# Kernel tuning notes

Hardware: AMD Instinct MI355X
Metric: run time of the kernel (lower is better)

Reference implementation:

```python
import jax, jax.numpy as jnp
import numpy as np

N, S, E, H = 8, 1024, 1024, 16
DK = E // H

def setup_inputs() -> dict:
    key = jax.random.key(0)
    ks = jax.random.split(key, 10)
    s = 1.0 / np.sqrt(E)
    x = jax.random.normal(ks[0], (N, S, E), dtype=jnp.float32)
    attn_mask = jax.random.randint(ks[1], (N, S, S), 0, 2) == 1
    Wq = jax.random.normal(ks[2], (E, E), dtype=jnp.float32) * s
    Wk = jax.random.normal(ks[3], (E, E), dtype=jnp.float32) * s
    Wv = jax.random.normal(ks[4], (E, E), dtype=jnp.float32) * s
    Wo = jax.random.normal(ks[5], (E, E), dtype=jnp.float32) * s
    bq = jax.random.normal(ks[6], (E,), dtype=jnp.float32) * s
    bk = jax.random.normal(ks[7], (E,), dtype=jnp.float32) * s
    bv = jax.random.normal(ks[8], (E,), dtype=jnp.float32) * s
    bo = jax.random.normal(ks[9], (E,), dtype=jnp.float32) * s
    return {"x": x, "attn_mask": attn_mask, "Wq": Wq, "bq": bq, "Wk": Wk, "bk": bk,
            "Wv": Wv, "bv": bv, "Wo": Wo, "bo": bo}

def reference(x, attn_mask, Wq, bq, Wk, bk, Wv, bv, Wo, bo):
    n, s, e = x.shape
    # projections, split into heads: (N, H, S, DK)
    q = (x @ Wq + bq).reshape(n, s, H, DK).transpose(0, 2, 1, 3)
    k = (x @ Wk + bk).reshape(n, s, H, DK).transpose(0, 2, 1, 3)
    v = (x @ Wv + bv).reshape(n, s, H, DK).transpose(0, 2, 1, 3)
    logits = jnp.einsum("nhqd,nhkd->nhqk", q, k) / np.sqrt(DK).astype(np.float32)
    # mask==True positions are suppressed (masked_fill with -1e9)
    logits = jnp.where(attn_mask[:, None, :, :], jnp.float32(-1e9), logits)
    attn = jax.nn.softmax(logits, axis=-1)  # exp(log_softmax) == softmax
    o = jnp.einsum("nhqk,nhkd->nhqd", attn, v)
    o = o.transpose(0, 2, 1, 3).reshape(n, s, e)
    return o @ Wo + bo
```

## Files before the change

kernel.cpp:

```cpp
#include <hip/hip_runtime.h>
#include <hip/hip_bf16.h>

typedef unsigned short u16;
typedef unsigned int   u32;
typedef unsigned long long u64;

#define SEQ 1024
#define EMB 1024
#define NH  16
#define DKH 64

#define QSCALE 0.18033688f
#define SCLAMP 43.3f

typedef __attribute__((ext_vector_type(8))) short short8;
typedef __attribute__((ext_vector_type(4))) float floatx4;

__device__ __forceinline__ float b2f(u16 u) {
  return __uint_as_float(((u32)u) << 16);
}
__device__ __forceinline__ u16 f2b(float f) {
  u32 u = __float_as_uint(f);
  u32 r = u + 0x7fffu + ((u >> 16) & 1u);
  return (u16)(r >> 16);
}

__device__ __forceinline__ void glds16(const u16* g, u16* l) {
  __builtin_amdgcn_global_load_lds(
      (const __attribute__((address_space(1))) u32*)g,
      (__attribute__((address_space(3))) u32*)l, 16, 0, 0);
}

__global__ __launch_bounds__(256) void probe_inputs(const u32* __restrict__ A,
                                                    const u32* __restrict__ B,
                                                    int* __restrict__ flags) {
  __shared__ int mA, mB, mBig, xB16;
  if (threadIdx.x == 0) { mA = 0; mB = 0; mBig = 0; xB16 = 0; }
  __syncthreads();
  int la = 0, lb = 0;
  for (int i = threadIdx.x; i < 4096; i += 256) {
    if ((A[i] & 0xFEFEFEFEu) == 0) la++;
    if ((B[i] & 0xFEFEFEFEu) == 0) lb++;
  }
  atomicAdd(&mA, la); atomicAdd(&mB, lb);
  __syncthreads();
  const int xIsB = (mA > mB) ? 1 : 0;
  const u32* X = xIsB ? B : A;
  const u32* M = xIsB ? A : B;
  int big = 0, cnt = 0;
  for (int i = threadIdx.x; i < 4096; i += 256)
    if (M[i] > 1u) big = 1;
  for (int i = threadIdx.x; i < 2048; i += 256) {
    u16 v = (u16)(X[i] & 0xffffu);
    int e = (v >> 7) & 0xFF;
    if (e >= 110 && e <= 135) cnt++;
  }
  if (big) atomicOr(&mBig, 1);
  atomicAdd(&xB16, cnt);
  __syncthreads();
  if (threadIdx.x == 0) {
    flags[0] = xIsB;
    flags[1] = (xB16 > 1500) ? 1 : 0;
    flags[2] = mBig;
  }
}

__global__ __launch_bounds__(256) void convert_x(const void* __restrict__ bigA,
                                                 const void* __restrict__ bigB,
                                                 const int* __restrict__ flags,
                                                 u16* __restrict__ out) {
  const void* x = flags[0] ? bigB : bigA;
  int i = (blockIdx.x * 256 + threadIdx.x) * 4;
  if (flags[1]) {
    *(ushort4*)(out + i) = *(const ushort4*)((const u16*)x + i);
  } else {
    float4 v = *(const float4*)((const float*)x + i);
    ushort4 o;
    o.x = f2b(v.x); o.y = f2b(v.y); o.z = f2b(v.z); o.w = f2b(v.w);
    *(ushort4*)(out + i) = o;
  }
}

__global__ __launch_bounds__(256) void build_maskbits(const void* __restrict__ bigA,
                                                      const void* __restrict__ bigB,
                                                      const int* __restrict__ flags,
                                                      u32* __restrict__ out) {
  const void* mask = flags[0] ? bigA : bigB;
  const int mbyte = flags[2];
  const int t = threadIdx.x;
  const int lane = t & 63, w = t >> 6;
  const u64 base0 = (u64)blockIdx.x * 8192;
#pragma unroll 4
  for (int k = 0; k < 32; k++) {
    u64 idx = base0 + k * 256 + t;
    int v;
    if (mbyte) v = ((const unsigned char*)mask)[idx] == 0;
    else       v = ((const u32*)mask)[idx] == 0;
    u64 b = __ballot(v);
    if (lane == 0) {
      u64 wbase = (base0 + k * 256 + w * 64) >> 5;
      out[wbase]     = (u32)b;
      out[wbase + 1] = (u32)(b >> 32);
    }
  }
}

__global__ __launch_bounds__(256) void transpose_convert_w4(
    const void* __restrict__ w0, const void* __restrict__ w1,
    const void* __restrict__ w2, const void* __restrict__ w3,
    u16* __restrict__ outQKV, u16* __restrict__ outO,
    const int* __restrict__ flags) {
  __shared__ float tile[32][33];
  const int z = blockIdx.z;
  const void* in = (z == 0) ? w0 : (z == 1) ? w1 : (z == 2) ? w2 : w3;
  u16* out = (z < 3) ? (outQKV + (u64)z * EMB * EMB) : outO;
  const float scale = (z == 0) ? QSCALE : 1.0f;
  const int amode = flags[1];
  const int tx = threadIdx.x & 31;
  const int ty = threadIdx.x >> 5;
  const int bx = blockIdx.x * 32, by = blockIdx.y * 32;
  if (amode) {
    const u16* inb = (const u16*)in;
#pragma unroll
    for (int r = ty; r < 32; r += 8)
      tile[r][tx] = b2f(inb[(u64)(by + r) * EMB + bx + tx]);
  } else {
    const float* inf = (const float*)in;
#pragma unroll
    for (int r = ty; r < 32; r += 8)
      tile[r][tx] = inf[(u64)(by + r) * EMB + bx + tx];
  }
  __syncthreads();
#pragma unroll
  for (int r = ty; r < 32; r += 8)
    out[(u64)(bx + r) * EMB + by + tx] = f2b(tile[tx][r] * scale);
}

__global__ __launch_bounds__(256) void convert_biases(const void* b0, const void* b1,
                                                      const void* b2, const void* b3,
                                                      float* __restrict__ out,
                                                      const int* __restrict__ flags) {
  const void* ptrs[4] = {b0, b1, b2, b3};
  const void* p = ptrs[blockIdx.x];
  const float scale = (blockIdx.x == 0) ? QSCALE : 1.0f;
  const int amode = flags[1];
  for (int i = threadIdx.x; i < 1024; i += 256) {
    float v = amode ? b2f(((const u16*)p)[i]) : ((const float*)p)[i];
    out[blockIdx.x * 1024 + i] = v * scale;
  }
}

#define VTP 65
__global__ __launch_bounds__(256) void transpose_v(const u16* __restrict__ in,
                                                   u16* __restrict__ out) {
  __shared__ u16 tile[64 * VTP];
  const int t = threadIdx.x;
  const int s0 = blockIdx.x * 64;
  const u64 off = (u64)blockIdx.y * SEQ * DKH;
  const int row = t >> 2, c0 = (t & 3) * 16;
  const u16* ip = in + off + (u64)(s0 + row) * DKH + c0;
  *(uint4*)(&tile[row * VTP + c0])     = *(const uint4*)(ip);
  *(uint4*)(&tile[row * VTP + c0 + 8]) = *(const uint4*)(ip + 8);
  __syncthreads();
  const int d = t >> 2;
  u16 buf[16];
#pragma unroll
  for (int j = 0; j < 16; j++) buf[j] = tile[(c0 + j) * VTP + d];
  u16* op = out + off + (u64)d * SEQ + s0 + c0;
  *(uint4*)(op)     = *(uint4*)(&buf[0]);
  *(uint4*)(op + 8) = *(uint4*)(&buf[8]);
}


template <int OUTMODE>
__device__ __forceinline__ void gemm_core(
    const u16* __restrict__ X, const u16* __restrict__ Wt,
    const float* __restrict__ bias,
    u16* __restrict__ Qg, u16* __restrict__ Kg, u16* __restrict__ Vh,
    float* __restrict__ outf, int row0) {
  __shared__ __align__(16) u16 lds[2][(256 + 128) * 64];
  const int t = threadIdx.x;
  const int lane = t & 63;
  const int w = t >> 6;
  const int wr = w >> 1, wc = w & 1;
  const int l15 = lane & 15, l4 = lane >> 4;
  const int bM = blockIdx.x * 256, bN = blockIdx.y * 128;
  const int r7 = l15 & 7;
  const int cA = (l4 ^ r7) << 3;
  const int cB = (l4 ^ r7 ^ 4) << 3;

  floatx4 acc[4][4];
#pragma unroll
  for (int i = 0; i < 4; i++)
#pragma unroll
    for (int j = 0; j < 4; j++)
      acc[i][j] = (floatx4){0.f, 0.f, 0.f, 0.f};

  const int srow = w * 8 + (lane >> 3);
  const int schk = ((lane & 7) ^ (lane >> 3)) << 3;
  const u16* Ap = X + (u64)(row0 + bM + srow) * EMB + schk;
  const u16* Bp = Wt + (u64)(bN + srow) * EMB + schk;
  u16* Ad0 = &lds[0][w * 512];
  u16* Bd0 = &lds[0][16384 + w * 512];
  u16* Ad1 = &lds[1][w * 512];
  u16* Bd1 = &lds[1][16384 + w * 512];

  auto stage = [&](u16* Ad, u16* Bd, int k0) {
    glds16(Ap + k0, Ad);
    glds16(Ap + k0 + 64 * EMB, Ad + 4096);
    glds16(Ap + k0 + 128 * EMB, Ad + 8192);
    glds16(Ap + k0 + 192 * EMB, Ad + 12288);
    glds16(Bp + k0, Bd);
    glds16(Bp + k0 + 64 * EMB, Bd + 4096);
  };

  auto compute = [&](const u16* __restrict__ Ab, const u16* __restrict__ Bb) {
    short8 bf[4][2];
#pragma unroll
    for (int n = 0; n < 4; n++) {
      const int gr = (wc * 64 + n * 16 + l15) * 64;
      bf[n][0] = *(const short8*)(&Bb[gr + cA]);
      bf[n][1] = *(const short8*)(&Bb[gr + cB]);
    }
#pragma unroll
    for (int mh = 0; mh < 2; mh++) {
      short8 af[2][2];
#pragma unroll
      for (int m = 0; m < 2; m++) {
        const int fr = (wr * 64 + mh * 32 + m * 16 + l15) * 64;
        af[m][0] = *(const short8*)(&Ab[fr + cA]);
        af[m][1] = *(const short8*)(&Ab[fr + cB]);
      }
      __builtin_amdgcn_s_setprio(1);
#pragma unroll
      for (int m = 0; m < 2; m++)
#pragma unroll
        for (int n = 0; n < 4; n++) {
          acc[mh * 2 + m][n] = __builtin_amdgcn_mfma_f32_16x16x32_bf16(
              af[m][0], bf[n][0], acc[mh * 2 + m][n], 0, 0, 0);
          acc[mh * 2 + m][n] = __builtin_amdgcn_mfma_f32_16x16x32_bf16(
              af[m][1], bf[n][1], acc[mh * 2 + m][n], 0, 0, 0);
        }
      __builtin_amdgcn_s_setprio(0);
    }
  };

  stage(Ad0, Bd0, 0);
  for (int k0 = 0; k0 < EMB; k0 += 128) {
    stage(Ad1, Bd1, k0 + 64);
    asm volatile("s_waitcnt vmcnt(6)" ::: "memory");
    asm volatile("s_barrier" ::: "memory");
    compute(&lds[0][0], &lds[0][16384]);
    asm volatile("s_barrier" ::: "memory");
    if (k0 + 128 < EMB) {
      stage(Ad0, Bd0, k0 + 128);
      asm volatile("s_waitcnt vmcnt(6)" ::: "memory");
    } else {
      asm volatile("s_waitcnt vmcnt(0)" ::: "memory");
    }
    asm volatile("s_barrier" ::: "memory");
    compute(&lds[1][0], &lds[1][16384]);
    asm volatile("s_barrier" ::: "memory");
  }

  if (OUTMODE == 0) {
    const int sec = bN >> 10;
    u16* outp = (sec == 0) ? Qg : (sec == 1) ? Kg : Vh;
#pragma unroll
    for (int n = 0; n < 4; n++) {
      int col = bN + wc * 64 + n * 16 + l15;
      float bv = bias[col];
      int colh = col & 1023;
      int h = colh >> 6, d = colh & 63;
#pragma unroll
      for (int mt = 0; mt < 4; mt++) {
#pragma unroll
        for (int r = 0; r < 4; r++) {
          int row = bM + wr * 64 + mt * 16 + l4 * 4 + r;
          float v = acc[mt][n][r] + bv;
          int nb = row >> 10, s = row & 1023;
          outp[((u64)((nb * NH + h) * SEQ + s)) * DKH + d] = f2b(v);
        }
      }
    }
  } else {
#pragma unroll
    for (int n = 0; n < 4; n++) {
      int col = bN + wc * 64 + n * 16 + l15;
      float bv = bias[col];
#pragma unroll
      for (int mt = 0; mt < 4; mt++) {
#pragma unroll
        for (int r = 0; r < 4; r++) {
          int row = bM + wr * 64 + mt * 16 + l4 * 4 + r;
          outf[(u64)row * EMB + col] = acc[mt][n][r] + bv;
        }
      }
    }
  }
}

__global__ __launch_bounds__(512, 2) void gemm_qkv(
    const u16* __restrict__ X, const u16* __restrict__ Wt,
    const float* __restrict__ bias,
    u16* __restrict__ Qg, u16* __restrict__ Kg, u16* __restrict__ Vh,
    int row0) {
  gemm_core<0>(X, Wt, bias, Qg, Kg, Vh, nullptr, row0);
}

__global__ __launch_bounds__(512, 2) void gemm_out(
    const u16* __restrict__ X, const u16* __restrict__ Wt,
    const float* __restrict__ bias, float* __restrict__ out) {
  gemm_core<1>(X, Wt, bias, nullptr, nullptr, nullptr, out, 0);
}

__global__ __launch_bounds__(512, 4) void attn_mfma(
    const u16* __restrict__ Q, const u16* __restrict__ K,
    const u16* __restrict__ Vt, const u32* __restrict__ maskbits,
    int b0, u16* __restrict__ ctx) {
  __shared__ __align__(16) u16 Ks[2][64 * 64];
  __shared__ __align__(16) u16 Vs[64 * 64];
  __shared__ __align__(16) u16 Ps[256 * 64];

  const int t = threadIdx.x;
  const int lane = t & 63, w = t >> 6;
  const int l15 = lane & 15, l4 = lane >> 4;
  const int bid = blockIdx.x;
  const int h = bid & 15;
  const int qt = (bid >> 4) & 3;
  const int n = bid >> 6;
  const int nh = n * NH + h;
  const int q0 = qt * 256;
  const u64 hoff = (u64)nh * SEQ * DKH;

  const int r7 = l15 & 7;
  const int cA = (l4 ^ r7) << 3;
  const int cB = (l4 ^ r7 ^ 4) << 3;

  const int rt = w * 8 + (lane >> 3);
  const int chk = ((lane & 7) ^ (lane >> 3)) << 3;
  const u16* Kp = K + hoff + (u64)rt * DKH + chk;
  const u16* Vp = Vt + hoff + (u64)rt * SEQ + chk;
  const int ldsO = w * 512;

  short8 qf[2][2];
  {
    const u16* qpA = Q + hoff + (u64)(q0 + w * 32 + l15) * DKH + l4 * 8;
    qf[0][0] = *(const short8*)(qpA);
    qf[0][1] = *(const short8*)(qpA + 32);
    const u16* qpB = qpA + 16 * DKH;
    qf[1][0] = *(const short8*)(qpB);
    qf[1][1] = *(const short8*)(qpB + 32);
  }

  short8 ones;
#pragma unroll
  for (int e = 0; e < 8; e++) ones[e] = (short)0x3F80;

  floatx4 o[2][4];
#pragma unroll
  for (int s = 0; s < 2; s++)
#pragma unroll
    for (int j = 0; j < 4; j++) o[s][j] = (floatx4){0.f, 0.f, 0.f, 0.f};
  floatx4 osum[2];
  osum[0] = (floatx4){0.f, 0.f, 0.f, 0.f};
  osum[1] = (floatx4){0.f, 0.f, 0.f, 0.f};

  const u64 mrow0 = ((u64)((b0 + n) * SEQ + q0 + w * 32 + l15)) * 32;
  const u64 mrow1 = mrow0 + 16 * 32;
  const int pq0 = w * 32 + l15;
  const int pq1 = pq0 + 16;
  const int pc0 = (l4 * 4) ^ (r7 << 3);

  glds16(Kp, &Ks[0][ldsO]);
  glds16(Vp, &Vs[ldsO]);
  __syncthreads();

  int cur = 0;
  for (int kc = 0; kc < SEQ; kc += 64) {
    if (kc > 0) glds16(Vp + kc, &Vs[ldsO]);
    const int havek = (kc + 64 < SEQ);
    if (havek) glds16(Kp + (kc + 64) * DKH, &Ks[cur ^ 1][ldsO]);

    const u64 mb0 = *(const u64*)(maskbits + mrow0 + (kc >> 5));
    const u64 mb1 = *(const u64*)(maskbits + mrow1 + (kc >> 5));
    const u16* Kc = &Ks[cur][0];

    __builtin_amdgcn_s_setprio(1);
#pragma unroll
    for (int j = 0; j < 4; j++) {
      const int rb = (j * 16 + l15) * 64;
      short8 kb0 = *(const short8*)(&Kc[rb + cA]);
      short8 kb1 = *(const short8*)(&Kc[rb + cB]);
      floatx4 s0 = (floatx4){0.f, 0.f, 0.f, 0.f};
      floatx4 s1 = (floatx4){0.f, 0.f, 0.f, 0.f};
      s0 = __builtin_amdgcn_mfma_f32_16x16x32_bf16(kb0, qf[0][0], s0, 0, 0, 0);
      s0 = __builtin_amdgcn_mfma_f32_16x16x32_bf16(kb1, qf[0][1], s0, 0, 0, 0);
      s1 = __builtin_amdgcn_mfma_f32_16x16x32_bf16(kb0, qf[1][0], s1, 0, 0, 0);
      s1 = __builtin_amdgcn_mfma_f32_16x16x32_bf16(kb1, qf[1][1], s1, 0, 0, 0);

      const u32 mj0 = (u32)(mb0 >> (j * 16 + l4 * 4));
      const u32 mj1 = (u32)(mb1 >> (j * 16 + l4 * 4));
      float p00 = __uint_as_float(
          __float_as_uint(__builtin_amdgcn_exp2f(fminf(s0[0], SCLAMP))) &
          (u32)__builtin_amdgcn_sbfe(mj0, 0, 1));
      float p01 = __uint_as_float(
          __float_as_uint(__builtin_amdgcn_exp2f(fminf(s0[1], SCLAMP))) &
          (u32)__builtin_amdgcn_sbfe(mj0, 1, 1));
      float p02 = __uint_as_float(
          __float_as_uint(__builtin_amdgcn_exp2f(fminf(s0[2], SCLAMP))) &
          (u32)__builtin_amdgcn_sbfe(mj0, 2, 1));
      float p03 = __uint_as_float(
          __float_as_uint(__builtin_amdgcn_exp2f(fminf(s0[3], SCLAMP))) &
          (u32)__builtin_amdgcn_sbfe(mj0, 3, 1));
      float p10 = __uint_as_float(
          __float_as_uint(__builtin_amdgcn_exp2f(fminf(s1[0], SCLAMP))) &
          (u32)__builtin_amdgcn_sbfe(mj1, 0, 1));
      float p11 = __uint_as_float(
          __float_as_uint(__builtin_amdgcn_exp2f(fminf(s1[1], SCLAMP))) &
          (u32)__builtin_amdgcn_sbfe(mj1, 1, 1));
      float p12 = __uint_as_float(
          __float_as_uint(__builtin_amdgcn_exp2f(fminf(s1[2], SCLAMP))) &
          (u32)__builtin_amdgcn_sbfe(mj1, 2, 1));
      float p13 = __uint_as_float(
          __float_as_uint(__builtin_amdgcn_exp2f(fminf(s1[3], SCLAMP))) &
          (u32)__builtin_amdgcn_sbfe(mj1, 3, 1));

      uint2 pk0, pk1;
      asm("v_cvt_pk_bf16_f32 %0, %1, %2" : "=v"(pk0.x) : "v"(p00), "v"(p01));
      asm("v_cvt_pk_bf16_f32 %0, %1, %2" : "=v"(pk0.y) : "v"(p02), "v"(p03));
      asm("v_cvt_pk_bf16_f32 %0, %1, %2" : "=v"(pk1.x) : "v"(p10), "v"(p11));
      asm("v_cvt_pk_bf16_f32 %0, %1, %2" : "=v"(pk1.y) : "v"(p12), "v"(p13));
      const int pcol = (j * 16) ^ pc0;
      *(uint2*)(&Ps[pq0 * 64 + pcol]) = pk0;
      *(uint2*)(&Ps[pq1 * 64 + pcol]) = pk1;
    }

    if (havek) asm volatile("s_waitcnt vmcnt(1)" ::: "memory");
    else       asm volatile("s_waitcnt vmcnt(0)" ::: "memory");
    __builtin_amdgcn_s_barrier();

    short8 pa[2][2];
    pa[0][0] = *(const short8*)(&Ps[pq0 * 64 + cA]);
    pa[0][1] = *(const short8*)(&Ps[pq0 * 64 + cB]);
    pa[1][0] = *(const short8*)(&Ps[pq1 * 64 + cA]);
    pa[1][1] = *(const short8*)(&Ps[pq1 * 64 + cB]);
#pragma unroll
    for (int j = 0; j < 4; j++) {
      const int rb = (j * 16 + l15) * 64;
      short8 vb0 = *(const short8*)(&Vs[rb + cA]);
      short8 vb1 = *(const short8*)(&Vs[rb + cB]);
      o[0][j] = __builtin_amdgcn_mfma_f32_16x16x32_bf16(pa[0][0], vb0, o[0][j], 0, 0, 0);
      o[0][j] = __builtin_amdgcn_mfma_f32_16x16x32_bf16(pa[0][1], vb1, o[0][j], 0, 0, 0);
      o[1][j] = __builtin_amdgcn_mfma_f32_16x16x32_bf16(pa[1][0], vb0, o[1][j], 0, 0, 0);
      o[1][j] = __builtin_amdgcn_mfma_f32_16x16x32_bf16(pa[1][1], vb1, o[1][j], 0, 0, 0);
    }
    osum[0] = __builtin_amdgcn_mfma_f32_16x16x32_bf16(pa[0][0], ones, osum[0], 0, 0, 0);
    osum[0] = __builtin_amdgcn_mfma_f32_16x16x32_bf16(pa[0][1], ones, osum[0], 0, 0, 0);
    osum[1] = __builtin_amdgcn_mfma_f32_16x16x32_bf16(pa[1][0], ones, osum[1], 0, 0, 0);
    osum[1] = __builtin_amdgcn_mfma_f32_16x16x32_bf16(pa[1][1], ones, osum[1], 0, 0, 0);
    __builtin_amdgcn_s_setprio(0);

    __syncthreads();
    cur ^= 1;
  }

#pragma unroll
  for (int s = 0; s < 2; s++) {
#pragma unroll
    for (int r = 0; r < 4; r++) {
      float invr = 1.0f / fmaxf(osum[s][r], 1e-30f);
      int q = q0 + w * 32 + s * 16 + l4 * 4 + r;
      u64 base = ((u64)(n * SEQ + q)) * EMB + h * DKH + l15;
#pragma unroll
      for (int j = 0; j < 4; j++)
        ctx[base + j * 16] = f2b(o[s][j][r] * invr);
    }
  }
}

extern "C" void kernel_launch(void* const* d_in, const int* in_sizes, int n_in,
                              void* d_out, int out_size, void* d_ws, size_t ws_size,
                              hipStream_t stream) {
  int bigI[2] = {0, 1}, wI[4] = {2, 4, 6, 8}, bI[4] = {3, 5, 7, 9};
  int nb = 0, nw = 0, nbi = 0;
  for (int i = 0; i < n_in; i++) {
    if (in_sizes[i] == 8388608) { if (nb < 2) bigI[nb++] = i; }
    else if (in_sizes[i] == 1048576) { if (nw < 4) wI[nw++] = i; }
    else if (in_sizes[i] == 1024) { if (nbi < 4) bI[nbi++] = i; }
  }
  int oq = 0, ok = 1, ov = 2, oo = 3;
  if (nb == 2 && bigI[0] == 4 && bigI[1] == 9) { oq = 2; ok = 0; ov = 3; oo = 1; }

  const void* bigA = d_in[bigI[0]];
  const void* bigB = d_in[bigI[1]];
  const void* Wq = d_in[wI[oq]];
  const void* Wk = d_in[wI[ok]];
  const void* Wv = d_in[wI[ov]];
  const void* Wo = d_in[wI[oo]];
  const void* bq = d_in[bI[oq]];
  const void* bk = d_in[bI[ok]];
  const void* bv = d_in[bI[ov]];
  const void* bo = d_in[bI[oo]];

  char* ws = (char*)d_ws;
  u16* WtQKV = (u16*)ws;
  u16* WtO   = (u16*)(ws + (6ull << 20));
  float* biasf = (float*)(ws + (8ull << 20));
  int* flags = (int*)(ws + (8ull << 20) + 16384);
  u32* maskbits = (u32*)(ws + (8ull << 20) + 65536);
  u16* xb = (u16*)(ws + (10ull << 20));
  char* grp = ws + (26ull << 20);

  int G = 1;
  for (int g = 8; g >= 1; g >>= 1) {
    if (ws_size >= (26ull << 20) + (u64)g * (8ull << 20)) { G = g; break; }
  }
  const u64 gsz = (u64)G * (2ull << 20);
  u16* Qg = (u16*)grp;
  u16* Kg = (u16*)(grp + gsz);
  u16* Vh = (u16*)(grp + 2 * gsz);
  u16* Vt = (u16*)(grp + 3 * gsz);

  dim3 tb(256);

  probe_inputs<<<dim3(1), tb, 0, stream>>>((const u32*)bigA, (const u32*)bigB, flags);
  convert_x<<<dim3(8192), tb, 0, stream>>>(bigA, bigB, flags, xb);
  build_maskbits<<<dim3(1024), tb, 0, stream>>>(bigA, bigB, flags, maskbits);

  transpose_convert_w4<<<dim3(32, 32, 4), tb, 0, stream>>>(Wq, Wk, Wv, Wo, WtQKV, WtO, flags);
  convert_biases<<<dim3(4), tb, 0, stream>>>(bq, bk, bv, bo, biasf, flags);

  for (int b0 = 0; b0 < 8; b0 += G) {
    int row0 = b0 * 1024;
    gemm_qkv<<<dim3(4 * G, 24), dim3(512), 0, stream>>>(xb, WtQKV, biasf, Qg, Kg, Vh, row0);
    transpose_v<<<dim3(16, G * 16), tb, 0, stream>>>(Vh, Vt);

    attn_mfma<<<dim3(G * 16 * 4), dim3(512), 0, stream>>>(Qg, Kg, Vt, maskbits, b0, Vh);

    gemm_out<<<dim3(4 * G, 8), dim3(512), 0, stream>>>(Vh, WtO, biasf + 3072,
                                                       (float*)d_out + (u64)row0 * EMB);
  }
}
```

Measured before the change: 317.2 us.

## Fuse V transpose into QKV GEMM epilogue and drop exp2 clamp

The QKV GEMM epilogue for the V section now stages the bf16 tile in LDS with an XOR swizzle and writes V directly in transposed (d, s) layout, which removes the separate transpose_v kernel and its round trip of V through global memory. The attention softmax also drops the fminf clamp before exp2. The fusion adds a barrier and LDS traffic to the V-section GEMM blocks. Removing the clamp saves one instruction per element but risks overflow to inf if a logit exceeds the exp2 range.

```diff
diff --git a/kernel.cpp b/kernel.cpp
--- a/kernel.cpp
+++ b/kernel.cpp
@@ -11,7 +11,6 @@
 #define DKH 64
 
 #define QSCALE 0.18033688f
-#define SCLAMP 43.3f
 
 typedef __attribute__((ext_vector_type(8))) short short8;
 typedef __attribute__((ext_vector_type(4))) float floatx4;
@@ -150,33 +149,12 @@
   }
 }
 
-#define VTP 65
-__global__ __launch_bounds__(256) void transpose_v(const u16* __restrict__ in,
-                                                   u16* __restrict__ out) {
-  __shared__ u16 tile[64 * VTP];
-  const int t = threadIdx.x;
-  const int s0 = blockIdx.x * 64;
-  const u64 off = (u64)blockIdx.y * SEQ * DKH;
-  const int row = t >> 2, c0 = (t & 3) * 16;
-  const u16* ip = in + off + (u64)(s0 + row) * DKH + c0;
-  *(uint4*)(&tile[row * VTP + c0])     = *(const uint4*)(ip);
-  *(uint4*)(&tile[row * VTP + c0 + 8]) = *(const uint4*)(ip + 8);
-  __syncthreads();
-  const int d = t >> 2;
-  u16 buf[16];
-#pragma unroll
-  for (int j = 0; j < 16; j++) buf[j] = tile[(c0 + j) * VTP + d];
-  u16* op = out + off + (u64)d * SEQ + s0 + c0;
-  *(uint4*)(op)     = *(uint4*)(&buf[0]);
-  *(uint4*)(op + 8) = *(uint4*)(&buf[8]);
-}
-
 
 template <int OUTMODE>
 __device__ __forceinline__ void gemm_core(
     const u16* __restrict__ X, const u16* __restrict__ Wt,
     const float* __restrict__ bias,
-    u16* __restrict__ Qg, u16* __restrict__ Kg, u16* __restrict__ Vh,
+    u16* __restrict__ Qg, u16* __restrict__ Kg, u16* __restrict__ Vt,
     float* __restrict__ outf, int row0) {
   __shared__ __align__(16) u16 lds[2][(256 + 128) * 64];
   const int t = threadIdx.x;
@@ -265,22 +243,56 @@
 
   if (OUTMODE == 0) {
     const int sec = bN >> 10;
-    u16* outp = (sec == 0) ? Qg : (sec == 1) ? Kg : Vh;
-#pragma unroll
-    for (int n = 0; n < 4; n++) {
-      int col = bN + wc * 64 + n * 16 + l15;
-      float bv = bias[col];
-      int colh = col & 1023;
-      int h = colh >> 6, d = colh & 63;
-#pragma unroll
-      for (int mt = 0; mt < 4; mt++) {
-#pragma unroll
-        for (int r = 0; r < 4; r++) {
-          int row = bM + wr * 64 + mt * 16 + l4 * 4 + r;
-          float v = acc[mt][n][r] + bv;
-          int nb = row >> 10, s = row & 1023;
-          outp[((u64)((nb * NH + h) * SEQ + s)) * DKH + d] = f2b(v);
+    if (sec < 2) {
+      u16* outp = (sec == 0) ? Qg : Kg;
+#pragma unroll
+      for (int n = 0; n < 4; n++) {
+        int col = bN + wc * 64 + n * 16 + l15;
+        float bv = bias[col];
+        int colh = col & 1023;
+        int h = colh >> 6, d = colh & 63;
+#pragma unroll
+        for (int mt = 0; mt < 4; mt++) {
+#pragma unroll
+          for (int r = 0; r < 4; r++) {
+            int row = bM + wr * 64 + mt * 16 + l4 * 4 + r;
+            float v = acc[mt][n][r] + bv;
+            int nb = row >> 10, s = row & 1023;
+            outp[((u64)((nb * NH + h) * SEQ + s)) * DKH + d] = f2b(v);
+          }
         }
+      }
+    } else {
+      u16* ldt = &lds[0][0];
+#pragma unroll
+      for (int n = 0; n < 4; n++) {
+        const int dl = wc * 64 + n * 16 + l15;
+        const float bv = bias[bN + dl];
+#pragma unroll
+        for (int mt = 0; mt < 4; mt++) {
+          const int sb = wr * 64 + mt * 16 + l4 * 4;
+          const int sp = sb ^ ((dl & 7) << 3);
+          u32 w0 = (u32)f2b(acc[mt][n][0] + bv) |
+                   ((u32)f2b(acc[mt][n][1] + bv) << 16);
+          u32 w1 = (u32)f2b(acc[mt][n][2] + bv) |
+                   ((u32)f2b(acc[mt][n][3] + bv) << 16);
+          *(u32*)(&ldt[dl * 256 + sp])     = w0;
+          *(u32*)(&ldt[dl * 256 + sp + 2]) = w1;
+        }
+      }
+      __syncthreads();
+      const int d  = t >> 2;
+      const int sq = (t & 3) * 64;
+      const int arow = row0 + bM;
+      const int nb = arow >> 10, s0 = arow & 1023;
+      const int h = ((bN & 1023) >> 6) + (d >> 6);
+      u16* vout = Vt + (u64)(nb * NH + h) * SEQ * DKH +
+                  (u64)(d & 63) * SEQ + s0 + sq;
+#pragma unroll
+      for (int c = 0; c < 8; c++) {
+        const int sc = sq + c * 8;
+        const int scs = sc ^ ((d & 7) << 3);
+        *(uint4*)(vout + c * 8) = *(const uint4*)(&ldt[d * 256 + scs]);
       }
     }
   } else {
@@ -303,9 +315,9 @@
 __global__ __launch_bounds__(512, 2) void gemm_qkv(
     const u16* __restrict__ X, const u16* __restrict__ Wt,
     const float* __restrict__ bias,
-    u16* __restrict__ Qg, u16* __restrict__ Kg, u16* __restrict__ Vh,
+    u16* __restrict__ Qg, u16* __restrict__ Kg, u16* __restrict__ Vt,
     int row0) {
-  gemm_core<0>(X, Wt, bias, Qg, Kg, Vh, nullptr, row0);
+  gemm_core<0>(X, Wt, bias, Qg, Kg, Vt, nullptr, row0);
 }
 
 __global__ __launch_bounds__(512, 2) void gemm_out(
@@ -402,28 +414,28 @@
       const u32 mj0 = (u32)(mb0 >> (j * 16 + l4 * 4));
       const u32 mj1 = (u32)(mb1 >> (j * 16 + l4 * 4));
       float p00 = __uint_as_float(
-          __float_as_uint(__builtin_amdgcn_exp2f(fminf(s0[0], SCLAMP))) &
+          __float_as_uint(__builtin_amdgcn_exp2f(s0[0])) &
           (u32)__builtin_amdgcn_sbfe(mj0, 0, 1));
       float p01 = __uint_as_float(
-          __float_as_uint(__builtin_amdgcn_exp2f(fminf(s0[1], SCLAMP))) &
+          __float_as_uint(__builtin_amdgcn_exp2f(s0[1])) &
           (u32)__builtin_amdgcn_sbfe(mj0, 1, 1));
       float p02 = __uint_as_float(
-          __float_as_uint(__builtin_amdgcn_exp2f(fminf(s0[2], SCLAMP))) &
+          __float_as_uint(__builtin_amdgcn_exp2f(s0[2])) &
           (u32)__builtin_amdgcn_sbfe(mj0, 2, 1));
       float p03 = __uint_as_float(
-          __float_as_uint(__builtin_amdgcn_exp2f(fminf(s0[3], SCLAMP))) &
+          __float_as_uint(__builtin_amdgcn_exp2f(s0[3])) &
           (u32)__builtin_amdgcn_sbfe(mj0, 3, 1));
       float p10 = __uint_as_float(
-          __float_as_uint(__builtin_amdgcn_exp2f(fminf(s1[0], SCLAMP))) &
+          __float_as_uint(__builtin_amdgcn_exp2f(s1[0])) &
           (u32)__builtin_amdgcn_sbfe(mj1, 0, 1));
       float p11 = __uint_as_float(
-          __float_as_uint(__builtin_amdgcn_exp2f(fminf(s1[1], SCLAMP))) &
+          __float_as_uint(__builtin_amdgcn_exp2f(s1[1])) &
           (u32)__builtin_amdgcn_sbfe(mj1, 1, 1));
       float p12 = __uint_as_float(
-          __float_as_uint(__builtin_amdgcn_exp2f(fminf(s1[2], SCLAMP))) &
+          __float_as_uint(__builtin_amdgcn_exp2f(s1[2])) &
           (u32)__builtin_amdgcn_sbfe(mj1, 2, 1));
       float p13 = __uint_as_float(
-          __float_as_uint(__builtin_amdgcn_exp2f(fminf(s1[3], SCLAMP))) &
+          __float_as_uint(__builtin_amdgcn_exp2f(s1[3])) &
           (u32)__builtin_amdgcn_sbfe(mj1, 3, 1));
 
       uint2 pk0, pk1;
@@ -519,7 +531,7 @@
   const u64 gsz = (u64)G * (2ull << 20);
   u16* Qg = (u16*)grp;
   u16* Kg = (u16*)(grp + gsz);
-  u16* Vh = (u16*)(grp + 2 * gsz);
+  u16* ctx = (u16*)(grp + 2 * gsz);
   u16* Vt = (u16*)(grp + 3 * gsz);
 
   dim3 tb(256);
@@ -533,12 +545,11 @@
 
   for (int b0 = 0; b0 < 8; b0 += G) {
     int row0 = b0 * 1024;
-    gemm_qkv<<<dim3(4 * G, 24), dim3(512), 0, stream>>>(xb, WtQKV, biasf, Qg, Kg, Vh, row0);
-    transpose_v<<<dim3(16, G * 16), tb, 0, stream>>>(Vh, Vt);
-
-    attn_mfma<<<dim3(G * 16 * 4), dim3(512), 0, stream>>>(Qg, Kg, Vt, maskbits, b0, Vh);
-
-    gemm_out<<<dim3(4 * G, 8), dim3(512), 0, stream>>>(Vh, WtO, biasf + 3072,
+    gemm_qkv<<<dim3(4 * G, 24), dim3(512), 0, stream>>>(xb, WtQKV, biasf, Qg, Kg, Vt, row0);
+
+    attn_mfma<<<dim3(G * 16 * 4), dim3(512), 0, stream>>>(Qg, Kg, Vt, maskbits, b0, ctx);
+
+    gemm_out<<<dim3(4 * G, 8), dim3(512), 0, stream>>>(ctx, WtO, biasf + 3072,
                                                        (float*)d_out + (u64)row0 * EMB);
   }
 }
```

New measurement: 304.4 us. 1.04x faster.
